# Performance work log

Hardware: AMD Instinct MI355X
Metric: run time of the kernel (lower is better)

## Reference

```python
import jax, jax.numpy as jnp
import numpy as np

S, B, H = 512, 64, 1024


def setup_inputs() -> dict:
    key = jax.random.key(0)
    ks = jax.random.split(key, 9)
    sc = 1.0 / np.sqrt(2 * H)
    return {
        "hidden": jax.random.normal(ks[0], (B, H), jnp.float32),
        "decoder_out": jax.random.normal(ks[1], (B, H), jnp.float32),
        "encoder_states": jax.random.normal(ks[2], (S, B, H), jnp.float32),
        "W_attn": jax.random.uniform(ks[3], (2 * H, 2 * H), jnp.float32, -sc, sc),
        "b_attn": jax.random.uniform(ks[4], (2 * H,), jnp.float32, -sc, sc),
        "W_attn2": jax.random.uniform(ks[5], (1, 2 * H), jnp.float32, -sc, sc),
        "b_attn2": jax.random.uniform(ks[6], (1,), jnp.float32, -sc, sc),
        "W_comb": jax.random.uniform(ks[7], (H, 2 * H), jnp.float32, -sc, sc),
        "b_comb": jax.random.uniform(ks[8], (H,), jnp.float32, -sc, sc),
    }


def reference(hidden, decoder_out, encoder_states, W_attn, b_attn, W_attn2, b_attn2, W_comb, b_comb):
    s, b, h = encoder_states.shape
    # per-timestep cat(hidden, enc_t) -> attn -> tanh -> attn2, fully batched over S
    hid = jnp.broadcast_to(hidden[None], (s, b, h))
    cat = jnp.concatenate([hid, encoder_states], axis=-1)            # [S,B,2H]
    scores = jnp.tanh(cat @ W_attn.T + b_attn) @ W_attn2.T + b_attn2  # [S,B,1]
    scores = scores[..., 0].T                                         # [B,S] (stack dim=1 + squeeze)
    attn_w = jax.nn.softmax(scores, axis=-1)                          # [B,S]
    # bmm([B,1,S], [B,S,H]) -> [B,H]
    applied = jnp.einsum("bs,sbh->bh", attn_w, encoder_states)
    out = jnp.concatenate([decoder_out, applied], axis=-1) @ W_comb.T + b_comb
    out = jnp.tanh(out)
    return out, applied
```

## Files before the change

kernel.cpp:

```cpp
#include <hip/hip_runtime.h>
#include <stdint.h>


typedef __attribute__((ext_vector_type(8))) short bf16x8;
typedef __attribute__((ext_vector_type(4))) float f32x4;

__device__ __forceinline__ float bf2f(uint16_t u) {
  return __uint_as_float(((uint32_t)u) << 16);
}
__device__ __forceinline__ uint16_t f2bf(float x) {
  uint32_t u = __float_as_uint(x);
  u += 0x7fffu + ((u >> 16) & 1u);
  return (uint16_t)(u >> 16);
}
__device__ __forceinline__ uint32_t pk2(float a, float b) {
  return (uint32_t)f2bf(a) | ((uint32_t)f2bf(b) << 16);
}
__device__ __forceinline__ uint4 cvt8(const float* __restrict__ p) {
  const float4 a = *(const float4*)p;
  const float4 b = *(const float4*)(p + 4);
  uint4 r;
  r.x = pk2(a.x, a.y); r.y = pk2(a.z, a.w);
  r.z = pk2(b.x, b.y); r.w = pk2(b.z, b.w);
  return r;
}
__device__ __forceinline__ float tanh_fast(float x) {
  const float e = __expf(2.f * x);
  return __builtin_fmaf(-2.f, __builtin_amdgcn_rcpf(e + 1.f), 1.f);
}
__device__ __forceinline__ void load16(const uint16_t* g, uint16_t* l) {
  __builtin_amdgcn_global_load_lds(
      (const __attribute__((address_space(1))) void*)g,
      (__attribute__((address_space(3))) void*)l, 16, 0, 0);
}

__global__ __launch_bounds__(256)
void cvt_gemmu_kernel(const float* __restrict__ enc, const float* __restrict__ Wa,
                      const float* __restrict__ Wc,
                      uint16_t* __restrict__ enc_bf, uint16_t* __restrict__ Wa_bf,
                      uint16_t* __restrict__ Wc_bf,
                      const float* __restrict__ hidden, float* __restrict__ U,
                      const float* __restrict__ ba) {
  __shared__ __align__(16) uint16_t sAB[2][128 * 32];
  const int t = threadIdx.x;
  if (blockIdx.x < 4608) {
    const int stride = 4608 * 256;
    for (int idx = blockIdx.x * 256 + t; idx < 4718592; idx += stride) {
      if (idx < 4194304) {
        ((uint4*)enc_bf)[idx] = cvt8(enc + (size_t)idx * 8);
      } else if (idx < 4456448) {
        const int k = idx - 4194304;
        const int j = k >> 7, c8 = k & 127;
        ((uint4*)Wa_bf)[k] = cvt8(Wa + (size_t)j * 2048 + 1024 + c8 * 8);
      } else {
        const int k = idx - 4456448;
        ((uint4*)Wc_bf)[k] = cvt8(Wc + (size_t)k * 8);
      }
    }
    return;
  }
  const int bx = blockIdx.x - 4608;
  uint16_t* sA = sAB[0];
  uint16_t* sB = sAB[1];
  const int lane = t & 63, wave = t >> 6;
  const int wm = wave >> 1, wn = wave & 1;
  const int bn0 = (bx & 15) * 128;
  const int kbase = (bx >> 4) * 256;
  const int srow = t >> 2, scol = (t & 3) * 8;
  const int ar0 = min(srow, 63), ar1 = min(64 + srow, 63);
  f32x4 acc[4][4];
#pragma unroll
  for (int i = 0; i < 4; ++i)
#pragma unroll
    for (int j = 0; j < 4; ++j) acc[i][j] = (f32x4){0.f, 0.f, 0.f, 0.f};
  const int mrow = wm * 64 + (lane & 15);
  const int nrow = wn * 64 + (lane & 15);
  const int kq = (lane >> 4) * 8;
  for (int kk = 0; kk < 8; ++kk) {
    const int k0 = kbase + (kk << 5);
    const uint4 va0 = cvt8(hidden + (size_t)ar0 * 1024 + scol + k0);
    const uint4 va1 = cvt8(hidden + (size_t)ar1 * 1024 + scol + k0);
    const uint4 vb0 = cvt8(Wa + (size_t)(bn0 + srow) * 2048 + scol + k0);
    const uint4 vb1 = cvt8(Wa + (size_t)(bn0 + 64 + srow) * 2048 + scol + k0);
    __syncthreads();
    *(uint4*)&sA[t * 8] = va0;
    *(uint4*)&sA[2048 + t * 8] = va1;
    *(uint4*)&sB[t * 8] = vb0;
    *(uint4*)&sB[2048 + t * 8] = vb1;
    __syncthreads();
    bf16x8 af[4], bfr[4];
#pragma unroll
    for (int i = 0; i < 4; ++i) af[i] = *(const bf16x8*)&sA[(mrow + i * 16) * 32 + kq];
#pragma unroll
    for (int j = 0; j < 4; ++j) bfr[j] = *(const bf16x8*)&sB[(nrow + j * 16) * 32 + kq];
#pragma unroll
    for (int i = 0; i < 4; ++i)
#pragma unroll
      for (int j = 0; j < 4; ++j)
        acc[i][j] = __builtin_amdgcn_mfma_f32_16x16x32_bf16(af[i], bfr[j], acc[i][j], 0, 0, 0);
  }
  const int colb = lane & 15, rquad = lane >> 4;
  const float bsc = (kbase == 0) ? 1.f : 0.f;
#pragma unroll
  for (int i = 0; i < 4; ++i)
#pragma unroll
    for (int r = 0; r < 4; ++r) {
      const int gm = wm * 64 + i * 16 + rquad * 4 + r;
      if (gm < 64) {
#pragma unroll
        for (int j = 0; j < 4; ++j) {
          const int gn = bn0 + wn * 64 + j * 16 + colb;
          atomicAdd(&U[gm * 2048 + gn], acc[i][j][r] + bsc * ba[gn]);
        }
      }
    }
}

__global__ __launch_bounds__(512, 2)
void gemm_score_kernel(const uint16_t* __restrict__ A,
                       const uint16_t* __restrict__ Bm,
                       float* __restrict__ outf,
                       const float* __restrict__ Ubias,
                       const float* __restrict__ bias) {
  __shared__ __align__(16) uint16_t lds[3][2][8192];

  const int t = threadIdx.x, lane = t & 63, wave = t >> 6;
  const int wm = wave >> 2, wn = wave & 3;
  const int wid = blockIdx.x;
  const int xcd = wid & 7, q = wid >> 3;
  const int bm0 = (xcd * 16 + (q >> 3)) * 256;
  const int bn0 = (q & 7) * 256;

  const uint16_t* gpA[2];
  const uint16_t* gpB[2];
  int sb[2];
#pragma unroll
  for (int qq = 0; qq < 2; ++qq) {
    const int s = qq * 512 + t;
    const int r = s >> 2, kc = s & 3;
    const int g = kc ^ ((r >> 1) & 3);
    gpA[qq] = A + (size_t)(bm0 + r) * 1024 + g * 8;
    gpB[qq] = Bm + (size_t)(bn0 + r) * 1024 + g * 8;
    sb[qq] = (qq * 512 + wave * 64) * 8;
  }

  f32x4 acc[8][4];
#pragma unroll
  for (int i = 0; i < 8; ++i)
#pragma unroll
    for (int j = 0; j < 4; ++j) acc[i][j] = (f32x4){0.f, 0.f, 0.f, 0.f};

  const int swz = ((lane >> 1) & 3) << 3;
  const int kq = ((lane >> 4) * 8) ^ swz;
  const int aoff = (wm * 128 + (lane & 15)) * 32 + kq;
  const int boff = (wn * 64 + (lane & 15)) * 32 + kq;

#pragma unroll
  for (int qq = 0; qq < 2; ++qq) {
    load16(gpA[qq], &lds[0][0][sb[qq]]);
    load16(gpB[qq], &lds[0][1][sb[qq]]);
  }
#pragma unroll
  for (int qq = 0; qq < 2; ++qq) {
    load16(gpA[qq] + 32, &lds[1][0][sb[qq]]);
    load16(gpB[qq] + 32, &lds[1][1][sb[qq]]);
  }
  asm volatile("s_waitcnt vmcnt(4)" ::: "memory");
  __builtin_amdgcn_s_barrier();

  constexpr int NT = 32;
#pragma unroll
  for (int kt = 0; kt < NT; ++kt) {
    const int bufc = kt % 3;
    if (kt + 2 < NT) {
      const int nb = (kt + 2) % 3;
      const int kpre = (kt + 2) * 32;
#pragma unroll
      for (int qq = 0; qq < 2; ++qq) {
        load16(gpA[qq] + kpre, &lds[nb][0][sb[qq]]);
        load16(gpB[qq] + kpre, &lds[nb][1][sb[qq]]);
      }
    }
    const uint16_t* sA = lds[bufc][0];
    const uint16_t* sB = lds[bufc][1];
    bf16x8 af[8], bfr[4];
#pragma unroll
    for (int i = 0; i < 8; ++i) af[i] = *(const bf16x8*)&sA[aoff + i * 512];
#pragma unroll
    for (int j = 0; j < 4; ++j) bfr[j] = *(const bf16x8*)&sB[boff + j * 512];
#pragma unroll
    for (int i = 0; i < 8; ++i)
#pragma unroll
      for (int j = 0; j < 4; ++j)
        acc[i][j] = __builtin_amdgcn_mfma_f32_16x16x32_bf16(af[i], bfr[j], acc[i][j], 0, 0, 0);
    if (kt + 2 < NT) {
      asm volatile("s_waitcnt vmcnt(4) lgkmcnt(0)" ::: "memory");
      __builtin_amdgcn_s_barrier();
    } else if (kt + 1 < NT) {
      asm volatile("s_waitcnt vmcnt(0) lgkmcnt(0)" ::: "memory");
      __builtin_amdgcn_s_barrier();
    }
  }

  const int colb = lane & 15, rquad = lane >> 4;
  float w2f[4];
#pragma unroll
  for (int j = 0; j < 4; ++j) w2f[j] = bias[bn0 + wn * 64 + j * 16 + colb];
#pragma unroll
  for (int i = 0; i < 8; ++i) {
#pragma unroll
    for (int r = 0; r < 4; ++r) {
      const int gm = bm0 + wm * 128 + i * 16 + rquad * 4 + r;
      const int bb = gm & 63;
      float p = 0.f;
#pragma unroll
      for (int j = 0; j < 4; ++j) {
        const float u = Ubias[bb * 2048 + bn0 + wn * 64 + j * 16 + colb];
        p += tanh_fast(acc[i][j][r] + u) * w2f[j];
      }
      p += __shfl_xor(p, 1);
      p += __shfl_xor(p, 2);
      p += __shfl_xor(p, 4);
      p += __shfl_xor(p, 8);
      if (colb == 0) atomicAdd(outf + gm, p);
    }
  }
}

__global__ __launch_bounds__(512)
void gemm_comb_kernel(const uint16_t* __restrict__ A,
                      const uint16_t* __restrict__ Bm,
                      float* __restrict__ outp,
                      const float* __restrict__ bias) {
  const int t = threadIdx.x, lane = t & 63, wave = t >> 6;
  const int g = blockIdx.x * 8 + wave;
  const int m0 = (g >> 6) * 16, n0 = (g & 63) * 16;
  const int rl = lane & 15, kq = (lane >> 4) * 8;
  const uint16_t* ap = A + (size_t)(m0 + rl) * 2048 + kq;
  const uint16_t* bp = Bm + (size_t)(n0 + rl) * 2048 + kq;
  f32x4 acc = (f32x4){0.f, 0.f, 0.f, 0.f};
#pragma unroll 8
  for (int ks = 0; ks < 64; ++ks) {
    const bf16x8 af = *(const bf16x8*)(ap + ks * 32);
    const bf16x8 bf = *(const bf16x8*)(bp + ks * 32);
    acc = __builtin_amdgcn_mfma_f32_16x16x32_bf16(af, bf, acc, 0, 0, 0);
  }
  const int gm = m0 + (lane >> 4) * 4;
  const int gn = n0 + rl;
  const float bj = bias[gn];
#pragma unroll
  for (int r = 0; r < 4; ++r)
    outp[(gm + r) * 1024 + gn] = tanh_fast(acc[r] + bj);
}

__global__ __launch_bounds__(256)
void applied_kernel(const uint16_t* __restrict__ encb, const float* __restrict__ dec,
                    const float* __restrict__ scores,
                    float* __restrict__ out_applied, uint16_t* __restrict__ acat) {
  const int b = blockIdx.x, chunk = blockIdx.y, t = threadIdx.x;
  const int wave = t >> 6, lane = t & 63;
  __shared__ float w[512];
  __shared__ float red[8];
  __shared__ float2 part2[256];
  float v0 = scores[(size_t)t * 64 + b];
  float v1 = scores[(size_t)(t + 256) * 64 + b];
  float mx = fmaxf(v0, v1);
#pragma unroll
  for (int off = 32; off >= 1; off >>= 1) mx = fmaxf(mx, __shfl_xor(mx, off));
  if (lane == 0) red[wave] = mx;
  __syncthreads();
  mx = fmaxf(fmaxf(red[0], red[1]), fmaxf(red[2], red[3]));
  const float e0 = __expf(v0 - mx), e1 = __expf(v1 - mx);
  float sum = e0 + e1;
#pragma unroll
  for (int off = 32; off >= 1; off >>= 1) sum += __shfl_xor(sum, off);
  if (lane == 0) red[4 + wave] = sum;
  __syncthreads();
  sum = (red[4] + red[5]) + (red[6] + red[7]);
  const float inv = 1.f / sum;
  w[t] = e0 * inv;
  w[t + 256] = e1 * inv;
  __syncthreads();
  const int hp = t & 31, sq = t >> 5;
  const int h = chunk * 64 + hp * 2;
  const uint32_t* base = (const uint32_t*)encb + (size_t)b * 512 + (h >> 1);
  float a0 = 0.f, a1 = 0.f;
#pragma unroll 8
  for (int s = sq * 64; s < sq * 64 + 64; ++s) {
    const uint32_t p = base[(size_t)s * 32768];
    a0 += w[s] * bf2f((uint16_t)(p & 0xffffu));
    a1 += w[s] * bf2f((uint16_t)(p >> 16));
  }
  part2[t] = make_float2(a0, a1);
  __syncthreads();
  if (t < 32) {
    a0 = 0.f; a1 = 0.f;
#pragma unroll
    for (int k = 0; k < 8; ++k) {
      const float2 pp = part2[t + 32 * k];
      a0 += pp.x; a1 += pp.y;
    }
    *(float2*)(out_applied + (size_t)b * 1024 + h) = make_float2(a0, a1);
    *(uint32_t*)(acat + (size_t)b * 2048 + 1024 + h) = pk2(a0, a1);
    *(uint32_t*)(acat + (size_t)b * 2048 + h) =
        pk2(dec[(size_t)b * 1024 + h], dec[(size_t)b * 1024 + h + 1]);
  }
}

extern "C" void kernel_launch(void* const* d_in, const int* in_sizes, int n_in,
                              void* d_out, int out_size, void* d_ws, size_t ws_size,
                              hipStream_t stream) {
  const float* hidden  = (const float*)d_in[0];
  const float* dec     = (const float*)d_in[1];
  const float* enc     = (const float*)d_in[2];
  const float* W_attn  = (const float*)d_in[3];
  const float* b_attn  = (const float*)d_in[4];
  const float* W_attn2 = (const float*)d_in[5];
  const float* W_comb  = (const float*)d_in[7];
  const float* b_comb  = (const float*)d_in[8];
  float* outp = (float*)d_out;

  char* ws = (char*)d_ws;
  float*    scores = (float*)(ws + 0);
  float*    U      = (float*)(ws + 131072);
  uint16_t* acat   = (uint16_t*)(ws + 655360);
  uint16_t* enc_bf = (uint16_t*)(ws + 1048576);
  uint16_t* Wa_bf  = (uint16_t*)(ws + 68157440);
  uint16_t* Wc_bf  = (uint16_t*)(ws + 72351744);

  hipMemsetAsync(ws, 0, 655360, stream);
  cvt_gemmu_kernel<<<4672, 256, 0, stream>>>(enc, W_attn, W_comb, enc_bf,
                                             Wa_bf, Wc_bf, hidden, U, b_attn);
  gemm_score_kernel<<<1024, 512, 0, stream>>>(enc_bf, Wa_bf, scores, U, W_attn2);
  applied_kernel<<<dim3(64, 16), 256, 0, stream>>>(enc_bf, dec, scores,
                                                   outp + 65536, acat);
  gemm_comb_kernel<<<32, 512, 0, stream>>>(acat, Wc_bf, outp, b_comb);
}
```

Baseline: 465.0 us.

## Load GEMM B operand directly from global into double-buffered registers

The B tile no longer goes through LDS. Each wave loads its MFMA B fragments straight from global memory into a two-slot register buffer, one k-step ahead; only the A tile stays in the triple-buffered LDS pipeline. The A fragment loads are also split into two halves to lower register pressure. This halves LDS use and removes the B-side LDS writes and reads, at the cost of redundant and poorly coalesced global reads of B across waves, plus more register-resident prefetch.

```diff
diff --git a/kernel.cpp b/kernel.cpp
--- a/kernel.cpp
+++ b/kernel.cpp
@@ -122,7 +122,7 @@
                        float* __restrict__ outf,
                        const float* __restrict__ Ubias,
                        const float* __restrict__ bias) {
-  __shared__ __align__(16) uint16_t lds[3][2][8192];
+  __shared__ __align__(16) uint16_t lds[3][8192];
 
   const int t = threadIdx.x, lane = t & 63, wave = t >> 6;
   const int wm = wave >> 2, wn = wave & 3;
@@ -132,7 +132,6 @@
   const int bn0 = (q & 7) * 256;
 
   const uint16_t* gpA[2];
-  const uint16_t* gpB[2];
   int sb[2];
 #pragma unroll
   for (int qq = 0; qq < 2; ++qq) {
@@ -140,9 +139,14 @@
     const int r = s >> 2, kc = s & 3;
     const int g = kc ^ ((r >> 1) & 3);
     gpA[qq] = A + (size_t)(bm0 + r) * 1024 + g * 8;
-    gpB[qq] = Bm + (size_t)(bn0 + r) * 1024 + g * 8;
     sb[qq] = (qq * 512 + wave * 64) * 8;
   }
+
+  const int rl = lane & 15, kq8 = (lane >> 4) * 8;
+  const uint16_t* gBf[4];
+#pragma unroll
+  for (int j = 0; j < 4; ++j)
+    gBf[j] = Bm + (size_t)(bn0 + wn * 64 + j * 16 + rl) * 1024 + kq8;
 
   f32x4 acc[8][4];
 #pragma unroll
@@ -152,49 +156,60 @@
 
   const int swz = ((lane >> 1) & 3) << 3;
   const int kq = ((lane >> 4) * 8) ^ swz;
-  const int aoff = (wm * 128 + (lane & 15)) * 32 + kq;
-  const int boff = (wn * 64 + (lane & 15)) * 32 + kq;
-
-#pragma unroll
-  for (int qq = 0; qq < 2; ++qq) {
-    load16(gpA[qq], &lds[0][0][sb[qq]]);
-    load16(gpB[qq], &lds[0][1][sb[qq]]);
-  }
-#pragma unroll
-  for (int qq = 0; qq < 2; ++qq) {
-    load16(gpA[qq] + 32, &lds[1][0][sb[qq]]);
-    load16(gpB[qq] + 32, &lds[1][1][sb[qq]]);
-  }
-  asm volatile("s_waitcnt vmcnt(4)" ::: "memory");
+  const int aoff = (wm * 128 + rl) * 32 + kq;
+
+  bf16x8 bfr[2][4];
+
+#pragma unroll
+  for (int qq = 0; qq < 2; ++qq) load16(gpA[qq], &lds[0][sb[qq]]);
+#pragma unroll
+  for (int j = 0; j < 4; ++j) bfr[0][j] = *(const bf16x8*)(gBf[j]);
+#pragma unroll
+  for (int qq = 0; qq < 2; ++qq) load16(gpA[qq] + 32, &lds[1][sb[qq]]);
+  asm volatile("s_waitcnt vmcnt(2)" ::: "memory");
   __builtin_amdgcn_s_barrier();
 
   constexpr int NT = 32;
 #pragma unroll
   for (int kt = 0; kt < NT; ++kt) {
     const int bufc = kt % 3;
+    if (kt + 1 < NT) {
+      const int ko = (kt + 1) * 32;
+#pragma unroll
+      for (int j = 0; j < 4; ++j)
+        bfr[(kt + 1) & 1][j] = *(const bf16x8*)(gBf[j] + ko);
+    }
     if (kt + 2 < NT) {
       const int nb = (kt + 2) % 3;
       const int kpre = (kt + 2) * 32;
 #pragma unroll
-      for (int qq = 0; qq < 2; ++qq) {
-        load16(gpA[qq] + kpre, &lds[nb][0][sb[qq]]);
-        load16(gpB[qq] + kpre, &lds[nb][1][sb[qq]]);
-      }
-    }
-    const uint16_t* sA = lds[bufc][0];
-    const uint16_t* sB = lds[bufc][1];
-    bf16x8 af[8], bfr[4];
-#pragma unroll
-    for (int i = 0; i < 8; ++i) af[i] = *(const bf16x8*)&sA[aoff + i * 512];
-#pragma unroll
-    for (int j = 0; j < 4; ++j) bfr[j] = *(const bf16x8*)&sB[boff + j * 512];
-#pragma unroll
-    for (int i = 0; i < 8; ++i)
-#pragma unroll
-      for (int j = 0; j < 4; ++j)
-        acc[i][j] = __builtin_amdgcn_mfma_f32_16x16x32_bf16(af[i], bfr[j], acc[i][j], 0, 0, 0);
+      for (int qq = 0; qq < 2; ++qq) load16(gpA[qq] + kpre, &lds[nb][sb[qq]]);
+    }
+    const uint16_t* sA = lds[bufc];
+    {
+      bf16x8 af[4];
+#pragma unroll
+      for (int i = 0; i < 4; ++i) af[i] = *(const bf16x8*)&sA[aoff + i * 512];
+#pragma unroll
+      for (int i = 0; i < 4; ++i)
+#pragma unroll
+        for (int j = 0; j < 4; ++j)
+          acc[i][j] = __builtin_amdgcn_mfma_f32_16x16x32_bf16(
+              af[i], bfr[kt & 1][j], acc[i][j], 0, 0, 0);
+    }
+    {
+      bf16x8 af[4];
+#pragma unroll
+      for (int i = 0; i < 4; ++i) af[i] = *(const bf16x8*)&sA[aoff + (i + 4) * 512];
+#pragma unroll
+      for (int i = 0; i < 4; ++i)
+#pragma unroll
+        for (int j = 0; j < 4; ++j)
+          acc[i + 4][j] = __builtin_amdgcn_mfma_f32_16x16x32_bf16(
+              af[i], bfr[kt & 1][j], acc[i + 4][j], 0, 0, 0);
+    }
     if (kt + 2 < NT) {
-      asm volatile("s_waitcnt vmcnt(4) lgkmcnt(0)" ::: "memory");
+      asm volatile("s_waitcnt vmcnt(2) lgkmcnt(0)" ::: "memory");
       __builtin_amdgcn_s_barrier();
     } else if (kt + 1 < NT) {
       asm volatile("s_waitcnt vmcnt(0) lgkmcnt(0)" ::: "memory");
```

Result: slower. 543.7 us (+16.9%).
